# Kernel tuning notes

Measured on AMD Instinct MI355X. Metric: run time of the kernel, lower is better.

## Reference

```python
import jax, jax.numpy as jnp
import numpy as np

N_NODES = 50000
N_EDGES = 800000
D_IN, D_HID, D_OUT = 128, 256, 256


def _sage_conv(x, src, dst, w_l, b_l, w_r, n_nodes):
    # PyG SAGEConv (mean aggr): out = lin_l(mean_{j in N(i)} x_j) + lin_r(x_i)
    # lin_l has bias, lin_r has no bias.
    msg_sum = jax.ops.segment_sum(x[src], dst, num_segments=n_nodes)  # [N, d]
    deg = jax.ops.segment_sum(jnp.ones_like(dst, dtype=x.dtype), dst, num_segments=n_nodes)
    agg = msg_sum / jnp.maximum(deg, 1.0)[:, None]
    return agg @ w_l.T + b_l + x @ w_r.T


def setup_inputs() -> dict:
    key = jax.random.key(0)
    ks = jax.random.split(key, 8)
    x = jax.random.normal(ks[0], (N_NODES, D_IN), dtype=jnp.float32)
    edge_index = jax.random.randint(ks[1], (2, N_EDGES), 0, N_NODES, dtype=jnp.int64)
    s1 = 1.0 / np.sqrt(D_IN)
    s2 = 1.0 / np.sqrt(D_HID)
    w_l1 = jax.random.uniform(ks[2], (D_HID, D_IN), jnp.float32, -s1, s1)
    b_l1 = jax.random.uniform(ks[3], (D_HID,), jnp.float32, -s1, s1)
    w_r1 = jax.random.uniform(ks[4], (D_HID, D_IN), jnp.float32, -s1, s1)
    w_l2 = jax.random.uniform(ks[5], (D_OUT, D_HID), jnp.float32, -s2, s2)
    b_l2 = jax.random.uniform(ks[6], (D_OUT,), jnp.float32, -s2, s2)
    w_r2 = jax.random.uniform(ks[7], (D_OUT, D_HID), jnp.float32, -s2, s2)
    return {"x": x, "edge_index": edge_index,
            "w_l1": w_l1, "b_l1": b_l1, "w_r1": w_r1,
            "w_l2": w_l2, "b_l2": b_l2, "w_r2": w_r2}


def reference(x, edge_index, w_l1, b_l1, w_r1, w_l2, b_l2, w_r2):
    src, dst = edge_index[0], edge_index[1]
    h = jax.nn.relu(_sage_conv(x, src, dst, w_l1, b_l1, w_r1, N_NODES))
    out = jax.nn.relu(_sage_conv(h, src, dst, w_l2, b_l2, w_r2, N_NODES))
    return out
```

## Files before the change

kernel.cpp:

```cpp
#include <hip/hip_runtime.h>
#include <hip/hip_fp16.h>
#include <stdint.h>

#define N_NODES 50000
#define N_EDGES 800000
#define BCAP 64
#define NPART 782
#define NSUB 4
#define SCAP 384

typedef _Float16 f16x8 __attribute__((ext_vector_type(8)));
typedef __attribute__((ext_vector_type(4))) float f32x4;

__device__ __forceinline__ unsigned short f2h(float f) {
    return __builtin_bit_cast(unsigned short, (_Float16)f);
}

__device__ __forceinline__ unsigned char f2fp8o(float v) {
    v = fminf(v, 440.f) + 0.015625f;
    unsigned int u = __builtin_bit_cast(unsigned int, v);
    u += 0x7FFFFu + ((u >> 20) & 1u);
    return (unsigned char)((u >> 20) - 960u);
}

__device__ __forceinline__ void load_lds16(const void* g, void* l) {
    __builtin_amdgcn_global_load_lds(
        (const __attribute__((address_space(1))) void*)(uintptr_t)g,
        (__attribute__((address_space(3))) void*)(unsigned int)(uintptr_t)l,
        16, 0, 0);
}

__global__ __launch_bounds__(256) void part_append_k(
    const int* __restrict__ src, const int* __restrict__ dst,
    int* __restrict__ pcnt, unsigned int* __restrict__ pbuf, int nedges)
{
    int e = blockIdx.x * 256 + threadIdx.x;
    if (e >= nedges) return;
    int s = src[e], d = dst[e];
    int cidx = (d >> 6) * NSUB + (e & (NSUB - 1));
    int pos = atomicAdd(&pcnt[cidx * 16], 1);
    if (pos < SCAP)
        pbuf[(size_t)cidx * SCAP + pos] = ((unsigned)(d & 63) << 16) | (unsigned)s;
}

__global__ __launch_bounds__(256) void part_bucket_k(
    const int* __restrict__ pcnt, const unsigned int* __restrict__ pbuf,
    int* __restrict__ bucket, int* __restrict__ degtot, float* __restrict__ invdeg)
{
    __shared__ int lcnt[64];
    int part = blockIdx.x, tid = threadIdx.x;
    if (tid < 64) lcnt[tid] = 0;
    __syncthreads();
#pragma unroll
    for (int sub = 0; sub < NSUB; sub++) {
        int cidx = part * NSUB + sub;
        int n = pcnt[cidx * 16];
        if (n > SCAP) n = SCAP;
        const unsigned int* pb = pbuf + (size_t)cidx * SCAP;
        for (int i = tid; i < n; i += 256) {
            unsigned int en = pb[i];
            int dlow = (int)(en >> 16), s = (int)(en & 0xFFFFu);
            int p = atomicAdd(&lcnt[dlow], 1);
            if (p < BCAP) bucket[(size_t)(part * 64 + dlow) * BCAP + p] = s;
        }
    }
    __syncthreads();
    if (tid < 64) {
        int node = part * 64 + tid;
        if (node < N_NODES) {
            int c = lcnt[tid];
            degtot[node] = (c > BCAP) ? BCAP : c;
            invdeg[node] = 1.0f / (float)(c > 1 ? c : 1);
        }
    }
}

__global__ __launch_bounds__(256) void cvt_x_k(
    const float* __restrict__ x, unsigned short* __restrict__ dst)
{
    int tid = blockIdx.x * 256 + threadIdx.x;
    if (tid >= N_NODES * 32) return;
    int row = tid >> 5, c = (tid & 31) * 4;
    float4 v = *(const float4*)(x + (size_t)row * 128 + c);
    ushort4 o;
    o.x = f2h(v.x); o.y = f2h(v.y); o.z = f2h(v.z); o.w = f2h(v.w);
    *(ushort4*)(dst + (size_t)row * 256 + 128 + c) = o;
}

__global__ __launch_bounds__(256) void cvt_w_k(
    const float* __restrict__ wl, const float* __restrict__ wr,
    unsigned short* __restrict__ dst, int Keach)
{
    int tid = blockIdx.x * 256 + threadIdx.x;
    if (tid >= 256 * 2 * Keach) return;
    int n = tid / (2 * Keach), k = tid - n * 2 * Keach;
    float v = (k < Keach) ? wl[(size_t)n * Keach + k]
                          : wr[(size_t)n * Keach + (k - Keach)];
    dst[tid] = f2h(v);
}

__device__ __forceinline__ void acch4(__half2* a, uint4 u) {
    a[0] = __hadd2(a[0], __builtin_bit_cast(__half2, u.x));
    a[1] = __hadd2(a[1], __builtin_bit_cast(__half2, u.y));
    a[2] = __hadd2(a[2], __builtin_bit_cast(__half2, u.z));
    a[3] = __hadd2(a[3], __builtin_bit_cast(__half2, u.w));
}

__global__ __launch_bounds__(256) void agg1_k(
    const unsigned short* __restrict__ feat,
    const int* __restrict__ bucket, const int* __restrict__ degtot,
    const float* __restrict__ invdeg,
    unsigned short* __restrict__ outmsg)
{
    int wv = threadIdx.x >> 6, lane = threadIdx.x & 63;
    int node = blockIdx.x * 4 + wv;
    if (node >= N_NODES) return;
    int deg = degtot[node];
    int idx0 = bucket[(size_t)node * BCAP + lane];
    const int sub = lane >> 4;
    const int col = lane & 15;

    __half2 acc[4] = {};
    auto rowp = [&](int s) { return (const uint4*)(feat + (size_t)s * 256 + col * 8); };

    int j = 0;
    for (; j + 16 <= deg; j += 16) {
        int s0 = __shfl(idx0, j + sub),     s1 = __shfl(idx0, j + 4 + sub);
        int s2 = __shfl(idx0, j + 8 + sub), s3 = __shfl(idx0, j + 12 + sub);
        uint4 u0 = *rowp(s0), u1 = *rowp(s1), u2 = *rowp(s2), u3 = *rowp(s3);
        acch4(acc, u0); acch4(acc, u1); acch4(acc, u2); acch4(acc, u3);
    }
    for (; j + 8 <= deg; j += 8) {
        int s0 = __shfl(idx0, j + sub), s1 = __shfl(idx0, j + 4 + sub);
        uint4 u0 = *rowp(s0), u1 = *rowp(s1);
        acch4(acc, u0); acch4(acc, u1);
    }
    for (; j + 4 <= deg; j += 4) {
        uint4 u0 = *rowp(__shfl(idx0, j + sub));
        acch4(acc, u0);
    }
    if (j < deg) {
        int e = j + sub;
        int ec = (e < deg) ? e : (deg - 1);
        uint4 u0 = *rowp(__shfl(idx0, ec));
        if (e < deg) acch4(acc, u0);
    }
#pragma unroll
    for (int stride = 32; stride >= 16; stride >>= 1)
#pragma unroll
        for (int v = 0; v < 4; v++) {
            int t = __shfl_xor(__builtin_bit_cast(int, acc[v]), stride);
            acc[v] = __hadd2(acc[v], __builtin_bit_cast(__half2, t));
        }

    if (lane < 16) {
        float s = invdeg[node];
        unsigned int o[4];
#pragma unroll
        for (int v = 0; v < 4; v++) {
            float2 f = __half22float2(acc[v]);
            o[v] = (unsigned int)f2h(f.x * s) | ((unsigned int)f2h(f.y * s) << 16);
        }
        *(uint4*)(outmsg + (size_t)node * 256 + lane * 8) = make_uint4(o[0], o[1], o[2], o[3]);
    }
}

__device__ __forceinline__ void accf8pk(__half2* a, unsigned int w) {
    unsigned int ev = ((w & 0x00FF00FFu) << 7) + 0x20002000u;
    unsigned int od = ((w >> 1) & 0x7F807F80u) + 0x20002000u;
    a[0] = __hadd2(a[0], __builtin_bit_cast(__half2, ev));
    a[1] = __hadd2(a[1], __builtin_bit_cast(__half2, od));
}
__device__ __forceinline__ void accf8x16(__half2* a, uint4 u) {
    accf8pk(a + 0, u.x); accf8pk(a + 2, u.y); accf8pk(a + 4, u.z); accf8pk(a + 6, u.w);
}

__global__ __launch_bounds__(256) void agg2_k(
    const unsigned char* __restrict__ hf8,
    const int* __restrict__ bucket, const int* __restrict__ degtot,
    const float* __restrict__ invdeg,
    unsigned short* __restrict__ outmsg)
{
    int wv = threadIdx.x >> 6, lane = threadIdx.x & 63;
    int node = blockIdx.x * 4 + wv;
    if (node >= N_NODES) return;
    int deg = degtot[node];
    int idx0 = bucket[(size_t)node * BCAP + lane];
    const int sub = lane >> 4;
    const int col = lane & 15;

    __half2 acc[8] = {};
    auto rowp = [&](int s) { return (const uint4*)(hf8 + (size_t)s * 256 + col * 16); };

    int j = 0;
    for (; j + 16 <= deg; j += 16) {
        int s0 = __shfl(idx0, j + sub),     s1 = __shfl(idx0, j + 4 + sub);
        int s2 = __shfl(idx0, j + 8 + sub), s3 = __shfl(idx0, j + 12 + sub);
        uint4 u0 = *rowp(s0), u1 = *rowp(s1), u2 = *rowp(s2), u3 = *rowp(s3);
        accf8x16(acc, u0); accf8x16(acc, u1); accf8x16(acc, u2); accf8x16(acc, u3);
    }
    for (; j + 8 <= deg; j += 8) {
        int s0 = __shfl(idx0, j + sub), s1 = __shfl(idx0, j + 4 + sub);
        uint4 u0 = *rowp(s0), u1 = *rowp(s1);
        accf8x16(acc, u0); accf8x16(acc, u1);
    }
    for (; j + 4 <= deg; j += 4) {
        uint4 u0 = *rowp(__shfl(idx0, j + sub));
        accf8x16(acc, u0);
    }
    if (j < deg) {
        int e = j + sub;
        int ec = (e < deg) ? e : (deg - 1);
        uint4 u0 = *rowp(__shfl(idx0, ec));
        if (e < deg) accf8x16(acc, u0);
    }
#pragma unroll
    for (int stride = 32; stride >= 16; stride >>= 1)
#pragma unroll
        for (int v = 0; v < 8; v++) {
            int t = __shfl_xor(__builtin_bit_cast(int, acc[v]), stride);
            acc[v] = __hadd2(acc[v], __builtin_bit_cast(__half2, t));
        }

    if (lane < 16) {
        float s = invdeg[node];
        float bias = (deg > 0) ? 0.015625f : 0.0f;
        unsigned int o[8];
#pragma unroll
        for (int q = 0; q < 4; q++) {
            float2 ev = __half22float2(acc[2 * q]);
            float2 od = __half22float2(acc[2 * q + 1]);
            float d0 = ev.x * s - bias, d1 = od.x * s - bias;
            float d2 = ev.y * s - bias, d3 = od.y * s - bias;
            o[2 * q]     = (unsigned int)f2h(d0) | ((unsigned int)f2h(d1) << 16);
            o[2 * q + 1] = (unsigned int)f2h(d2) | ((unsigned int)f2h(d3) << 16);
        }
        unsigned short* wp = outmsg + (size_t)node * 512 + lane * 16;
        *(uint4*)(wp)     = make_uint4(o[0], o[1], o[2], o[3]);
        *(uint4*)(wp + 8) = make_uint4(o[4], o[5], o[6], o[7]);
    }
}

template <bool F16OUT, bool WRITE_FP8>
__global__ __launch_bounds__(256) void gemm_k(
    const unsigned short* __restrict__ A, const unsigned short* __restrict__ W,
    const float* __restrict__ bias, void* __restrict__ outp, int outStride,
    unsigned char* __restrict__ hf8, int M, int K)
{
    __shared__ __align__(16) char smem[2 * 16384];
    const int t = threadIdx.x;
    const int w = t >> 6, lane = t & 63;
    const int quad = lane >> 4, l15 = lane & 15;
    const int row0 = blockIdx.x * 128;
    const int col0 = blockIdx.y * 128;
    const int niter = K >> 5;

    auto stage = [&](int buf, int ks) {
#pragma unroll
        for (int j = 0; j < 4; j++) {
            int call = w * 4 + j;
            int ci = call * 64 + lane;
            const unsigned short* g;
            if (call < 8) {
                int rg = row0 + (ci >> 2);
                if (rg > M - 1) rg = M - 1;
                g = A + (size_t)rg * K + ks + (ci & 3) * 8;
            } else {
                int c2 = ci - 512;
                g = W + (size_t)(col0 + (c2 >> 2)) * K + ks + (c2 & 3) * 8;
            }
            load_lds16(g, smem + buf * 16384 + ci * 16);
        }
    };

    f32x4 acc[2][8] = {};

    stage(0, 0);
    __syncthreads();

    for (int i = 0; i < niter; i++) {
        if (i + 1 < niter) stage((i + 1) & 1, (i + 1) << 5);

        const char* base = smem + (i & 1) * 16384;
        const char* Ab = base + (w * 32 + l15) * 64 + quad * 16;
        const char* Wb = base + 8192 + l15 * 64 + quad * 16;
        f16x8 af0 = *(const f16x8*)(Ab);
        f16x8 af1 = *(const f16x8*)(Ab + 1024);
#pragma unroll
        for (int tt = 0; tt < 8; tt++) {
            f16x8 bfr = *(const f16x8*)(Wb + tt * 1024);
            acc[0][tt] = __builtin_amdgcn_mfma_f32_16x16x32_f16(af0, bfr, acc[0][tt], 0, 0, 0);
            acc[1][tt] = __builtin_amdgcn_mfma_f32_16x16x32_f16(af1, bfr, acc[1][tt], 0, 0, 0);
        }
        __syncthreads();
    }

#pragma unroll
    for (int g = 0; g < 2; g++) {
#pragma unroll
        for (int tt = 0; tt < 8; tt++) {
            int col = col0 + tt * 16 + l15;
            float bv = bias[col];
#pragma unroll
            for (int i = 0; i < 4; i++) {
                int row = row0 + w * 32 + g * 16 + quad * 4 + i;
                if (row < M) {
                    float v = fmaxf(acc[g][tt][i] + bv, 0.f);
                    size_t off = (size_t)row * outStride + col;
                    if constexpr (F16OUT) ((unsigned short*)outp)[off] = f2h(v);
                    else                  ((float*)outp)[off] = v;
                    if constexpr (WRITE_FP8) hf8[(size_t)row * 256 + col] = f2fp8o(v);
                }
            }
        }
    }
}

extern "C" void kernel_launch(void* const* d_in, const int* in_sizes, int n_in,
                              void* d_out, int out_size, void* d_ws, size_t ws_size,
                              hipStream_t stream)
{
    const float* x   = (const float*)d_in[0];
    const int*   ei  = (const int*)d_in[1];
    const float* wl1 = (const float*)d_in[2];
    const float* bl1 = (const float*)d_in[3];
    const float* wr1 = (const float*)d_in[4];
    const float* wl2 = (const float*)d_in[5];
    const float* bl2 = (const float*)d_in[6];
    const float* wr2 = (const float*)d_in[7];
    float* out = (float*)d_out;
    const int* src = ei;
    const int* dst = ei + N_EDGES;

    char* ws = (char*)d_ws;
    size_t off = 0;
    auto alloc = [&](size_t bytes) -> void* {
        void* p = ws + off;
        off = (off + bytes + 255) & ~(size_t)255;
        return p;
    };
    int*            pcnt   = (int*)           alloc((size_t)NPART * NSUB * 16 * 4);
    unsigned int*   pbuf   = (unsigned int*)  alloc((size_t)NPART * NSUB * SCAP * 4);
    int*            bucket = (int*)           alloc((size_t)NPART * 64 * BCAP * 4);
    int*            degtot = (int*)           alloc((size_t)N_NODES * 4);
    float*          invdeg = (float*)         alloc((size_t)N_NODES * 4);
    unsigned short* Acat1  = (unsigned short*)alloc((size_t)N_NODES * 256 * 2);
    unsigned short* Acat2  = (unsigned short*)alloc((size_t)N_NODES * 512 * 2);
    unsigned char*  hf8    = (unsigned char*) alloc((size_t)N_NODES * 256);
    unsigned short* Wcat1  = (unsigned short*)alloc((size_t)256 * 256 * 2);
    unsigned short* Wcat2  = (unsigned short*)alloc((size_t)256 * 512 * 2);

    hipMemsetAsync(pcnt, 0, (size_t)NPART * NSUB * 16 * 4, stream);
    part_append_k<<<(N_EDGES + 255) / 256, 256, 0, stream>>>(src, dst, pcnt, pbuf, N_EDGES);
    part_bucket_k<<<NPART, 256, 0, stream>>>(pcnt, pbuf, bucket, degtot, invdeg);

    cvt_x_k<<<(N_NODES * 32 + 255) / 256, 256, 0, stream>>>(x, Acat1);
    cvt_w_k<<<(256 * 256 + 255) / 256, 256, 0, stream>>>(wl1, wr1, Wcat1, 128);
    cvt_w_k<<<(256 * 512 + 255) / 256, 256, 0, stream>>>(wl2, wr2, Wcat2, 256);

    agg1_k<<<(N_NODES + 3) / 4, 256, 0, stream>>>(
        Acat1 + 128, bucket, degtot, invdeg, Acat1);
    gemm_k<true, true><<<dim3((N_NODES + 127) / 128, 2), 256, 0, stream>>>(
        Acat1, Wcat1, bl1, (void*)(Acat2 + 256), 512, hf8, N_NODES, 256);

    agg2_k<<<(N_NODES + 3) / 4, 256, 0, stream>>>(
        hf8, bucket, degtot, invdeg, Acat2);
    gemm_k<false, false><<<dim3((N_NODES + 127) / 128, 2), 256, 0, stream>>>(
        Acat2, Wcat2, bl2, (void*)out, 256, nullptr, N_NODES, 512);
}
```

Baseline: 279.4 us.

## Keep full W tile resident in swizzled LDS, stream A from registers, widen edge partitioning

The GEMM now loads the whole 64-column weight slice for all K into LDS once, using an XOR swizzle to avoid bank conflicts. A fragments are read straight from global memory into registers with one-step prefetch, which replaces the per-step double-buffered A/W LDS staging and its barriers. The grid is doubled to four column blocks of 64. The edge partition kernel handles four edges per thread with vector loads and uses 16 sub-buckets of 128 entries to spread atomic contention, and the bucket kernel gives each wave its own sub-bucket. In exchange, A is re-read once per column block, the K=512 variant uses 64 KB of LDS, which limits occupancy, and the smaller sub-bucket capacity raises the risk of overflow drops.

```diff
diff --git a/kernel.cpp b/kernel.cpp
--- a/kernel.cpp
+++ b/kernel.cpp
@@ -6,8 +6,8 @@
 #define N_EDGES 800000
 #define BCAP 64
 #define NPART 782
-#define NSUB 4
-#define SCAP 384
+#define NSUB 16
+#define SCAP 128
 
 typedef _Float16 f16x8 __attribute__((ext_vector_type(8)));
 typedef __attribute__((ext_vector_type(4))) float f32x4;
@@ -34,13 +34,26 @@
     const int* __restrict__ src, const int* __restrict__ dst,
     int* __restrict__ pcnt, unsigned int* __restrict__ pbuf, int nedges)
 {
-    int e = blockIdx.x * 256 + threadIdx.x;
-    if (e >= nedges) return;
-    int s = src[e], d = dst[e];
-    int cidx = (d >> 6) * NSUB + (e & (NSUB - 1));
-    int pos = atomicAdd(&pcnt[cidx * 16], 1);
-    if (pos < SCAP)
-        pbuf[(size_t)cidx * SCAP + pos] = ((unsigned)(d & 63) << 16) | (unsigned)s;
+    int t = blockIdx.x * 256 + threadIdx.x;
+    int e0 = t * 4;
+    if (e0 >= nedges) return;
+    int4 s4 = *(const int4*)(src + e0);
+    int4 d4 = *(const int4*)(dst + e0);
+
+    int c0 = (d4.x >> 6) * NSUB + ((e0 + 0) & (NSUB - 1));
+    int c1 = (d4.y >> 6) * NSUB + ((e0 + 1) & (NSUB - 1));
+    int c2 = (d4.z >> 6) * NSUB + ((e0 + 2) & (NSUB - 1));
+    int c3 = (d4.w >> 6) * NSUB + ((e0 + 3) & (NSUB - 1));
+
+    int p0 = atomicAdd(&pcnt[c0 * 16], 1);
+    int p1 = atomicAdd(&pcnt[c1 * 16], 1);
+    int p2 = atomicAdd(&pcnt[c2 * 16], 1);
+    int p3 = atomicAdd(&pcnt[c3 * 16], 1);
+
+    if (p0 < SCAP) pbuf[(size_t)c0 * SCAP + p0] = ((unsigned)(d4.x & 63) << 16) | (unsigned)s4.x;
+    if (p1 < SCAP) pbuf[(size_t)c1 * SCAP + p1] = ((unsigned)(d4.y & 63) << 16) | (unsigned)s4.y;
+    if (p2 < SCAP) pbuf[(size_t)c2 * SCAP + p2] = ((unsigned)(d4.z & 63) << 16) | (unsigned)s4.z;
+    if (p3 < SCAP) pbuf[(size_t)c3 * SCAP + p3] = ((unsigned)(d4.w & 63) << 16) | (unsigned)s4.w;
 }
 
 __global__ __launch_bounds__(256) void part_bucket_k(
@@ -49,15 +62,16 @@
 {
     __shared__ int lcnt[64];
     int part = blockIdx.x, tid = threadIdx.x;
+    int wv = tid >> 6, lane = tid & 63;
     if (tid < 64) lcnt[tid] = 0;
     __syncthreads();
 #pragma unroll
-    for (int sub = 0; sub < NSUB; sub++) {
+    for (int sub = wv; sub < NSUB; sub += 4) {
         int cidx = part * NSUB + sub;
         int n = pcnt[cidx * 16];
         if (n > SCAP) n = SCAP;
         const unsigned int* pb = pbuf + (size_t)cidx * SCAP;
-        for (int i = tid; i < n; i += 256) {
+        for (int i = lane; i < n; i += 64) {
             unsigned int en = pb[i];
             int dlow = (int)(en >> 16), s = (int)(en & 0xFFFFu);
             int p = atomicAdd(&lcnt[dlow], 1);
@@ -241,64 +255,72 @@
     }
 }
 
-template <bool F16OUT, bool WRITE_FP8>
+template <bool F16OUT, bool WRITE_FP8, int K>
 __global__ __launch_bounds__(256) void gemm_k(
     const unsigned short* __restrict__ A, const unsigned short* __restrict__ W,
     const float* __restrict__ bias, void* __restrict__ outp, int outStride,
-    unsigned char* __restrict__ hf8, int M, int K)
-{
-    __shared__ __align__(16) char smem[2 * 16384];
+    unsigned char* __restrict__ hf8, int M)
+{
+    constexpr int NITER = K / 32;
+    constexpr int KC = K / 8;
+    __shared__ __align__(16) char smem[64 * K * 2];
+
     const int t = threadIdx.x;
     const int w = t >> 6, lane = t & 63;
     const int quad = lane >> 4, l15 = lane & 15;
     const int row0 = blockIdx.x * 128;
-    const int col0 = blockIdx.y * 128;
-    const int niter = K >> 5;
-
-    auto stage = [&](int buf, int ks) {
-#pragma unroll
-        for (int j = 0; j < 4; j++) {
-            int call = w * 4 + j;
-            int ci = call * 64 + lane;
-            const unsigned short* g;
-            if (call < 8) {
-                int rg = row0 + (ci >> 2);
-                if (rg > M - 1) rg = M - 1;
-                g = A + (size_t)rg * K + ks + (ci & 3) * 8;
-            } else {
-                int c2 = ci - 512;
-                g = W + (size_t)(col0 + (c2 >> 2)) * K + ks + (c2 & 3) * 8;
-            }
-            load_lds16(g, smem + buf * 16384 + ci * 16);
-        }
-    };
-
-    f32x4 acc[2][8] = {};
-
-    stage(0, 0);
+    const int col0 = blockIdx.y * 64;
+
+    for (int c = t; c < 64 * KC; c += 256) {
+        int col = c / KC;
+        int kc  = (c % KC) ^ (col & 7);
+        load_lds16(W + (size_t)(col0 + col) * K + kc * 8, smem + c * 16);
+    }
+
+    int r0 = row0 + w * 32 + l15;      if (r0 > M - 1) r0 = M - 1;
+    int r1 = row0 + w * 32 + 16 + l15; if (r1 > M - 1) r1 = M - 1;
+    const unsigned short* pA0 = A + (size_t)r0 * K + quad * 8;
+    const unsigned short* pA1 = A + (size_t)r1 * K + quad * 8;
+
+    f16x8 a0c, a1c, a0n, a1n;
+    a0c = *(const f16x8*)(pA0);
+    a1c = *(const f16x8*)(pA1);
+
     __syncthreads();
 
-    for (int i = 0; i < niter; i++) {
-        if (i + 1 < niter) stage((i + 1) & 1, (i + 1) << 5);
-
-        const char* base = smem + (i & 1) * 16384;
-        const char* Ab = base + (w * 32 + l15) * 64 + quad * 16;
-        const char* Wb = base + 8192 + l15 * 64 + quad * 16;
-        f16x8 af0 = *(const f16x8*)(Ab);
-        f16x8 af1 = *(const f16x8*)(Ab + 1024);
-#pragma unroll
-        for (int tt = 0; tt < 8; tt++) {
-            f16x8 bfr = *(const f16x8*)(Wb + tt * 1024);
-            acc[0][tt] = __builtin_amdgcn_mfma_f32_16x16x32_f16(af0, bfr, acc[0][tt], 0, 0, 0);
-            acc[1][tt] = __builtin_amdgcn_mfma_f32_16x16x32_f16(af1, bfr, acc[1][tt], 0, 0, 0);
-        }
-        __syncthreads();
+    const int qs = (quad * 16) ^ ((l15 & 7) << 4);
+    const char* wp0 = smem + (size_t)(0 * 16 + l15) * (2 * K);
+    const char* wp1 = smem + (size_t)(1 * 16 + l15) * (2 * K);
+    const char* wp2 = smem + (size_t)(2 * 16 + l15) * (2 * K);
+    const char* wp3 = smem + (size_t)(3 * 16 + l15) * (2 * K);
+
+    f32x4 acc[2][4] = {};
+
+    for (int i = 0; i < NITER; i++) {
+        if (i + 1 < NITER) {
+            a0n = *(const f16x8*)(pA0 + (i + 1) * 32);
+            a1n = *(const f16x8*)(pA1 + (i + 1) * 32);
+        }
+        const int off = (i * 64) ^ qs;
+        f16x8 b0 = *(const f16x8*)(wp0 + off);
+        f16x8 b1 = *(const f16x8*)(wp1 + off);
+        f16x8 b2 = *(const f16x8*)(wp2 + off);
+        f16x8 b3 = *(const f16x8*)(wp3 + off);
+        acc[0][0] = __builtin_amdgcn_mfma_f32_16x16x32_f16(a0c, b0, acc[0][0], 0, 0, 0);
+        acc[1][0] = __builtin_amdgcn_mfma_f32_16x16x32_f16(a1c, b0, acc[1][0], 0, 0, 0);
+        acc[0][1] = __builtin_amdgcn_mfma_f32_16x16x32_f16(a0c, b1, acc[0][1], 0, 0, 0);
+        acc[1][1] = __builtin_amdgcn_mfma_f32_16x16x32_f16(a1c, b1, acc[1][1], 0, 0, 0);
+        acc[0][2] = __builtin_amdgcn_mfma_f32_16x16x32_f16(a0c, b2, acc[0][2], 0, 0, 0);
+        acc[1][2] = __builtin_amdgcn_mfma_f32_16x16x32_f16(a1c, b2, acc[1][2], 0, 0, 0);
+        acc[0][3] = __builtin_amdgcn_mfma_f32_16x16x32_f16(a0c, b3, acc[0][3], 0, 0, 0);
+        acc[1][3] = __builtin_amdgcn_mfma_f32_16x16x32_f16(a1c, b3, acc[1][3], 0, 0, 0);
+        a0c = a0n; a1c = a1n;
     }
 
 #pragma unroll
     for (int g = 0; g < 2; g++) {
 #pragma unroll
-        for (int tt = 0; tt < 8; tt++) {
+        for (int tt = 0; tt < 4; tt++) {
             int col = col0 + tt * 16 + l15;
             float bv = bias[col];
 #pragma unroll
@@ -351,7 +373,7 @@
     unsigned short* Wcat2  = (unsigned short*)alloc((size_t)256 * 512 * 2);
 
     hipMemsetAsync(pcnt, 0, (size_t)NPART * NSUB * 16 * 4, stream);
-    part_append_k<<<(N_EDGES + 255) / 256, 256, 0, stream>>>(src, dst, pcnt, pbuf, N_EDGES);
+    part_append_k<<<(N_EDGES / 4 + 255) / 256, 256, 0, stream>>>(src, dst, pcnt, pbuf, N_EDGES);
     part_bucket_k<<<NPART, 256, 0, stream>>>(pcnt, pbuf, bucket, degtot, invdeg);
 
     cvt_x_k<<<(N_NODES * 32 + 255) / 256, 256, 0, stream>>>(x, Acat1);
@@ -360,11 +382,11 @@
 
     agg1_k<<<(N_NODES + 3) / 4, 256, 0, stream>>>(
         Acat1 + 128, bucket, degtot, invdeg, Acat1);
-    gemm_k<true, true><<<dim3((N_NODES + 127) / 128, 2), 256, 0, stream>>>(
-        Acat1, Wcat1, bl1, (void*)(Acat2 + 256), 512, hf8, N_NODES, 256);
+    gemm_k<true, true, 256><<<dim3((N_NODES + 127) / 128, 4), 256, 0, stream>>>(
+        Acat1, Wcat1, bl1, (void*)(Acat2 + 256), 512, hf8, N_NODES);
 
     agg2_k<<<(N_NODES + 3) / 4, 256, 0, stream>>>(
         hf8, bucket, degtot, invdeg, Acat2);
-    gemm_k<false, false><<<dim3((N_NODES + 127) / 128, 2), 256, 0, stream>>>(
-        Acat2, Wcat2, bl2, (void*)out, 256, nullptr, N_NODES, 512);
-}
+    gemm_k<false, false, 512><<<dim3((N_NODES + 127) / 128, 4), 256, 0, stream>>>(
+        Acat2, Wcat2, bl2, (void*)out, 256, nullptr, N_NODES);
+}
```

Result: slower. 292.4 us (+4.6%).
